# Performance work log

Hardware: AMD Instinct MI355X
Metric: run time of the kernel (lower is better)

The kernel has to match this reference:

```python
import jax, jax.numpy as jnp
import numpy as np
from jax import lax

N = 64          # n (even -> odd=0, add_odd=0)
B = 256         # batch
F = 256         # input_features
ITERS = 10      # sinkhorn iterations


def _conv1d(x, w, b, pad, dil):
    # x: (B, Cin, L), w: (Cout, Cin, K) torch layout
    y = lax.conv_general_dilated(
        x, w, window_strides=(1,), padding=[(pad, pad)],
        rhs_dilation=(dil,), dimension_numbers=("NCH", "OIH", "NCH"))
    return y + b[None, :, None]


def setup_inputs() -> dict:
    key = jax.random.key(0)
    ks = jax.random.split(key, 17)
    s = 0.02
    d = {
        "x": jax.random.normal(ks[0], (B, F), jnp.float32),
        # linear stack (torch Linear layout: (out, in))
        "w1": jax.random.normal(ks[1], (2 * N, F), jnp.float32) * s,
        "b1": jax.random.normal(ks[2], (2 * N,), jnp.float32) * s,
        "w2": jax.random.normal(ks[3], (N * N, 2 * N), jnp.float32) * s,
        "b2": jax.random.normal(ks[4], (N * N,), jnp.float32) * s,
        "w3": jax.random.normal(ks[5], (4 * N * N, N * N), jnp.float32) * s,
        "b3": jax.random.normal(ks[6], (4 * N * N,), jnp.float32) * s,
        # conv stack: 2n->3n->2n->n->n->n, all k=3
        "cw1": jax.random.normal(ks[7], (3 * N, 2 * N, 3), jnp.float32) * s,
        "cb1": jax.random.normal(ks[8], (3 * N,), jnp.float32) * s,
        "cw2": jax.random.normal(ks[9], (2 * N, 3 * N, 3), jnp.float32) * s,
        "cb2": jax.random.normal(ks[10], (2 * N,), jnp.float32) * s,
        "cw3": jax.random.normal(ks[11], (N, 2 * N, 3), jnp.float32) * s,
        "cb3": jax.random.normal(ks[12], (N,), jnp.float32) * s,
        "cw4": jax.random.normal(ks[13], (N, N, 3), jnp.float32) * s,
        "cb4": jax.random.normal(ks[14], (N,), jnp.float32) * s,
        "cw5": jax.random.normal(ks[15], (N, N, 3), jnp.float32) * s,
        "cb5": jax.random.normal(ks[16], (N,), jnp.float32) * s,
    }
    return d


def _sink(x, iters):
    # output = x + 0.001; repeat: row-normalize then col-normalize
    out = x + 0.001

    def body(o, _):
        o = o / jnp.sum(o, axis=2, keepdims=True)  # row_sink: divide each row by its sum
        o = o / jnp.sum(o, axis=1, keepdims=True)  # col_sink: divide each column by its sum
        return o, None

    out, _ = lax.scan(body, out, None, length=iters)
    return out


def reference(x, w1, b1, w2, b2, w3, b3,
              cw1, cb1, cw2, cb2, cw3, cb3, cw4, cb4, cw5, cb5):
    h = x @ w1.T + b1
    h = h @ w2.T + b2
    h = h @ w3.T + b3                      # (B, 4n^2)
    h = h.reshape(B, 2 * N, 2 * N)         # (B, 128, 128)
    # conv1: p=0, d=(n-8)//2=28 (since n>10); rest pad=0, dil=1
    h = _conv1d(h, cw1, cb1, 0, (N - 8) // 2)  # (B, 192, 72)
    h = _conv1d(h, cw2, cb2, 0, 1)             # (B, 128, 70)
    h = _conv1d(h, cw3, cb3, 0, 1)             # (B, 64, 68)
    h = _conv1d(h, cw4, cb4, 0, 1)             # (B, 64, 66)
    h = _conv1d(h, cw5, cb5, 0, 1)             # (B, 64, 64)
    h = h * h                                   # torch.pow(x, 2)
    return _sink(h, ITERS)
```

## Files before the change

kernel.cpp:

```cpp
#include <hip/hip_runtime.h>
#include <hip/hip_bf16.h>

typedef float f32x4 __attribute__((ext_vector_type(4)));
typedef __bf16 bf16x8 __attribute__((ext_vector_type(8)));

__global__ __launch_bounds__(128) void gemm1_k(const float* __restrict__ x,
                                               const float* __restrict__ w1,
                                               const float* __restrict__ b1,
                                               float* __restrict__ h1) {
    __shared__ float xs[256];
    const int m = blockIdx.x, t = threadIdx.x;
    xs[t] = x[m * 256 + t];
    xs[t + 128] = x[m * 256 + 128 + t];
    __syncthreads();
    float acc = b1[t];
    const float4* wr = (const float4*)(w1 + t * 256);
#pragma unroll 8
    for (int k4 = 0; k4 < 64; ++k4) {
        float4 w = wr[k4];
        acc += xs[k4 * 4 + 0] * w.x + xs[k4 * 4 + 1] * w.y +
               xs[k4 * 4 + 2] * w.z + xs[k4 * 4 + 3] * w.w;
    }
    h1[m * 128 + t] = acc;
}

__global__ __launch_bounds__(256) void gemm2_k(const float* __restrict__ h1,
                                               const float* __restrict__ w2,
                                               const float* __restrict__ b2,
                                               float* __restrict__ h2) {
    __shared__ float As[64][129];
    __shared__ float Bs[64][129];
    const int nb = blockIdx.x, mb = blockIdx.y, t = threadIdx.x;
#pragma unroll
    for (int i = 0; i < 8; ++i) {
        int idx = i * 256 + t;
        int row = idx >> 5, c4 = (idx & 31) * 4;
        float4 a = *(const float4*)(h1 + (mb * 64 + row) * 128 + c4);
        As[row][c4 + 0] = a.x; As[row][c4 + 1] = a.y;
        As[row][c4 + 2] = a.z; As[row][c4 + 3] = a.w;
        float4 bv = *(const float4*)(w2 + (nb * 64 + row) * 128 + c4);
        Bs[row][c4 + 0] = bv.x; Bs[row][c4 + 1] = bv.y;
        Bs[row][c4 + 2] = bv.z; Bs[row][c4 + 3] = bv.w;
    }
    __syncthreads();
    const int tx = t & 15, ty = t >> 4;
    float acc[4][4] = {};
#pragma unroll 4
    for (int k = 0; k < 128; ++k) {
        float a[4], b[4];
#pragma unroll
        for (int i = 0; i < 4; ++i) a[i] = As[ty * 4 + i][k];
#pragma unroll
        for (int j = 0; j < 4; ++j) b[j] = Bs[tx * 4 + j][k];
#pragma unroll
        for (int i = 0; i < 4; ++i)
#pragma unroll
            for (int j = 0; j < 4; ++j) acc[i][j] += a[i] * b[j];
    }
#pragma unroll
    for (int i = 0; i < 4; ++i)
#pragma unroll
        for (int j = 0; j < 4; ++j) {
            int n = nb * 64 + tx * 4 + j;
            h2[(mb * 64 + ty * 4 + i) * 4096 + n] = acc[i][j] + b2[n];
        }
}

__device__ __forceinline__ void g3_load(const float* __restrict__ A,
                                        const float* __restrict__ W,
                                        int n0, int k0, int tid,
                                        float4 (&ar)[4][2], float4 (&wr)[2]) {
    const int kb = tid & 7, mrow = tid >> 3;
#pragma unroll
    for (int i = 0; i < 4; ++i) {
        const float* p = A + (i * 64 + mrow) * 4096 + k0 + kb * 8;
        ar[i][0] = *(const float4*)p;
        ar[i][1] = *(const float4*)(p + 4);
    }
    const float* q = W + (n0 + mrow) * 4096 + k0 + kb * 8;
    wr[0] = *(const float4*)q;
    wr[1] = *(const float4*)(q + 4);
}

__device__ __forceinline__ bf16x8 pack8(const float4& lo, const float4& hi) {
    bf16x8 p;
    p[0] = (__bf16)lo.x; p[1] = (__bf16)lo.y; p[2] = (__bf16)lo.z; p[3] = (__bf16)lo.w;
    p[4] = (__bf16)hi.x; p[5] = (__bf16)hi.y; p[6] = (__bf16)hi.z; p[7] = (__bf16)hi.w;
    return p;
}

__device__ __forceinline__ void g3_store(char* Ab, char* Wb, int tid,
                                         const float4 (&ar)[4][2],
                                         const float4 (&wr)[2]) {
    const int kb = tid & 7, mrow = tid >> 3;
#pragma unroll
    for (int i = 0; i < 4; ++i) {
        int m = i * 64 + mrow;
        *(bf16x8*)(Ab + ((m * 128 + kb * 16) ^ ((m & 7) << 4))) = pack8(ar[i][0], ar[i][1]);
    }
    *(bf16x8*)(Wb + ((mrow * 128 + kb * 16) ^ ((mrow & 7) << 4))) = pack8(wr[0], wr[1]);
}

__global__ __launch_bounds__(512, 1) void gemm3_k(const float* __restrict__ A,
                                                  const float* __restrict__ W,
                                                  const float* __restrict__ bias,
                                                  float* __restrict__ C) {
    __shared__ __align__(16) char lds[81920];
    const int tid = threadIdx.x;
    const int n0 = blockIdx.x * 64;

    float4 ar[4][2];
    float4 wr[2];
    g3_load(A, W, n0, 0, tid, ar, wr);
    g3_store(lds, lds + 65536, tid, ar, wr);
    __syncthreads();

    const int lane = tid & 63, wid = tid >> 6;
    const int lr = lane & 15, lq = lane >> 4;
    const int wm = wid >> 1, wn = wid & 1;

    f32x4 acc[4][2];
    const f32x4 zero = {0.f, 0.f, 0.f, 0.f};
#pragma unroll
    for (int mi = 0; mi < 4; ++mi)
#pragma unroll
        for (int ni = 0; ni < 2; ++ni) acc[mi][ni] = zero;

    for (int t = 0; t < 64; ++t) {
        const int cur = t & 1;
        if (t < 63) g3_load(A, W, n0, (t + 1) * 64, tid, ar, wr);
        const char* Ac = lds + cur * 32768;
        const char* Wc = lds + 65536 + cur * 8192;
#pragma unroll
        for (int kk = 0; kk < 2; ++kk) {
            const int kb = kk * 4 + lq;
            bf16x8 af[4], bfv[2];
#pragma unroll
            for (int mi = 0; mi < 4; ++mi) {
                int m = wm * 64 + mi * 16 + lr;
                af[mi] = *(const bf16x8*)(Ac + ((m * 128 + kb * 16) ^ ((m & 7) << 4)));
            }
#pragma unroll
            for (int ni = 0; ni < 2; ++ni) {
                int n = wn * 32 + ni * 16 + lr;
                bfv[ni] = *(const bf16x8*)(Wc + ((n * 128 + kb * 16) ^ ((n & 7) << 4)));
            }
#pragma unroll
            for (int mi = 0; mi < 4; ++mi)
#pragma unroll
                for (int ni = 0; ni < 2; ++ni)
                    acc[mi][ni] = __builtin_amdgcn_mfma_f32_16x16x32_bf16(
                        af[mi], bfv[ni], acc[mi][ni], 0, 0, 0);
        }
        __syncthreads();
        if (t < 63)
            g3_store(lds + (cur ^ 1) * 32768, lds + 65536 + (cur ^ 1) * 8192,
                     tid, ar, wr);
        __syncthreads();
    }

    float bv[2];
#pragma unroll
    for (int ni = 0; ni < 2; ++ni) bv[ni] = bias[n0 + wn * 32 + ni * 16 + lr];
#pragma unroll
    for (int mi = 0; mi < 4; ++mi)
#pragma unroll
        for (int ni = 0; ni < 2; ++ni) {
            const int n = n0 + wn * 32 + ni * 16 + lr;
#pragma unroll
            for (int r = 0; r < 4; ++r) {
                int m = wm * 64 + mi * 16 + lq * 4 + r;
                C[m * 16384 + n] = acc[mi][ni][r] + bv[ni];
            }
        }
}

template <int CIN, int COUT, int DIL, int MT, int NT>
__device__ __forceinline__ void conv_core(const char* xt, char* wl,
                                          const float* __restrict__ w,
                                          f32x4 (&acc)[MT][NT], int tid) {
    constexpr int RB = CIN * 2;
    const int lane = tid & 63, wid = tid >> 6;
    const int lr = lane & 15, lq = lane >> 4;
    const int cobase = wid * (COUT / 4);
    const f32x4 zero = {0.f, 0.f, 0.f, 0.f};
#pragma unroll
    for (int mi = 0; mi < MT; ++mi)
#pragma unroll
        for (int ni = 0; ni < NT; ++ni) acc[mi][ni] = zero;

    for (int cic = 0; cic < CIN / 32; ++cic) {
        for (int idx = tid; idx < COUT * 4; idx += 256) {
            int co = idx >> 2, cib = idx & 3, ci0 = cic * 32 + cib * 8;
            const float* src = w + co * (CIN * 3) + ci0 * 3;
            float v[24];
#pragma unroll
            for (int u = 0; u < 6; ++u) {
                float4 f = *(const float4*)(src + u * 4);
                v[u * 4 + 0] = f.x; v[u * 4 + 1] = f.y;
                v[u * 4 + 2] = f.z; v[u * 4 + 3] = f.w;
            }
#pragma unroll
            for (int tp = 0; tp < 3; ++tp) {
                bf16x8 pk;
#pragma unroll
                for (int j = 0; j < 8; ++j) pk[j] = (__bf16)v[j * 3 + tp];
                *(bf16x8*)(wl + ((tp * 4 + cib) * COUT + co) * 16) = pk;
            }
        }
        __syncthreads();
#pragma unroll
        for (int tp = 0; tp < 3; ++tp) {
            bf16x8 af[MT];
#pragma unroll
            for (int mi = 0; mi < MT; ++mi)
                af[mi] = *(const bf16x8*)(wl + ((tp * 4 + lq) * COUT + cobase + mi * 16 + lr) * 16);
            bf16x8 bfr[NT];
#pragma unroll
            for (int ni = 0; ni < NT; ++ni) {
                int colX = ni * 16 + lr + tp * DIL;
                bfr[ni] = *(const bf16x8*)(xt + ((colX * RB + (cic * 4 + lq) * 16) ^ ((colX & 7) << 4)));
            }
#pragma unroll
            for (int mi = 0; mi < MT; ++mi)
#pragma unroll
                for (int ni = 0; ni < NT; ++ni)
                    acc[mi][ni] = __builtin_amdgcn_mfma_f32_16x16x32_bf16(
                        af[mi], bfr[ni], acc[mi][ni], 0, 0, 0);
        }
        __syncthreads();
    }
}

template <int COUT, int LOUT, int MT, int NT>
__device__ __forceinline__ void write_xt(char* xt_out, const f32x4 (&acc)[MT][NT],
                                         const float* __restrict__ bias, int tid) {
    constexpr int RBO = COUT * 2;
    const int lane = tid & 63, wid = tid >> 6;
    const int lr = lane & 15, lq = lane >> 4;
    const int cobase = wid * (COUT / 4);
#pragma unroll
    for (int mi = 0; mi < MT; ++mi)
#pragma unroll
        for (int ni = 0; ni < NT; ++ni) {
            int l = ni * 16 + lr;
            if (l < LOUT) {
#pragma unroll
                for (int r = 0; r < 4; ++r) {
                    int co = cobase + mi * 16 + lq * 4 + r;
                    float y = acc[mi][ni][r] + bias[co];
                    int byte = (l * RBO + ((co >> 3) << 4) + (co & 7) * 2) ^ ((l & 7) << 4);
                    *(__bf16*)(xt_out + byte) = (__bf16)y;
                }
            }
        }
}

__global__ __launch_bounds__(256, 1) void convsink_k(
    const float* __restrict__ h3,
    const float* __restrict__ cw1, const float* __restrict__ cb1,
    const float* __restrict__ cw2, const float* __restrict__ cb2,
    const float* __restrict__ cw3, const float* __restrict__ cb3,
    const float* __restrict__ cw4, const float* __restrict__ cb4,
    const float* __restrict__ cw5, const float* __restrict__ cb5,
    float* __restrict__ out) {
    __shared__ __align__(16) char lds[34816 + 31488 + 36864 + 16640];
    char* xtA = lds;
    char* xtB = lds + 34816;
    char* wl = lds + 34816 + 31488;
    float* S = (float*)(lds + 34816 + 31488 + 36864);

    const int b = blockIdx.x, tid = threadIdx.x;
    const float* src = h3 + b * 16384;

#pragma unroll
    for (int i = 0; i < 8; ++i) {
        int idx = i * 256 + tid;
        int l = idx & 127, cib = idx >> 7;
        bf16x8 p;
#pragma unroll
        for (int j = 0; j < 8; ++j) p[j] = (__bf16)src[(cib * 8 + j) * 128 + l];
        *(bf16x8*)(xtA + ((l * 256 + cib * 16) ^ ((l & 7) << 4))) = p;
    }
    __syncthreads();

    {
        f32x4 acc[3][5];
        conv_core<128, 192, 28, 3, 5>(xtA, wl, cw1, acc, tid);
        write_xt<192, 72, 3, 5>(xtB, acc, cb1, tid);
    }
    __syncthreads();
    {
        f32x4 acc[2][5];
        conv_core<192, 128, 1, 2, 5>(xtB, wl, cw2, acc, tid);
        write_xt<128, 70, 2, 5>(xtA, acc, cb2, tid);
    }
    __syncthreads();
    {
        f32x4 acc[1][5];
        conv_core<128, 64, 1, 1, 5>(xtA, wl, cw3, acc, tid);
        write_xt<64, 68, 1, 5>(xtB, acc, cb3, tid);
    }
    __syncthreads();
    {
        f32x4 acc[1][5];
        conv_core<64, 64, 1, 1, 5>(xtB, wl, cw4, acc, tid);
        write_xt<64, 66, 1, 5>(xtA, acc, cb4, tid);
    }
    __syncthreads();
    {
        f32x4 acc[1][4];
        conv_core<64, 64, 1, 1, 4>(xtA, wl, cw5, acc, tid);
        const int lane = tid & 63, wid = tid >> 6;
        const int lr = lane & 15, lq = lane >> 4;
        const int cobase = wid * 16;
#pragma unroll
        for (int ni = 0; ni < 4; ++ni) {
            int l = ni * 16 + lr;
#pragma unroll
            for (int r = 0; r < 4; ++r) {
                int co = cobase + lq * 4 + r;
                float y = acc[0][ni][r] + cb5[co];
                S[co * 65 + l] = y * y + 0.001f;
            }
        }
    }
    __syncthreads();

    const int q = tid & 3, rid = tid >> 2;
    for (int it = 0; it < 10; ++it) {
        float p = 0.f;
#pragma unroll
        for (int j = 0; j < 16; ++j) p += S[rid * 65 + q * 16 + j];
        p += __shfl_xor(p, 1);
        p += __shfl_xor(p, 2);
        float inv = 1.0f / p;
#pragma unroll
        for (int j = 0; j < 16; ++j) S[rid * 65 + q * 16 + j] *= inv;
        __syncthreads();
        float c = 0.f;
#pragma unroll
        for (int i = 0; i < 16; ++i) c += S[(q * 16 + i) * 65 + rid];
        c += __shfl_xor(c, 1);
        c += __shfl_xor(c, 2);
        float invc = 1.0f / c;
#pragma unroll
        for (int i = 0; i < 16; ++i) S[(q * 16 + i) * 65 + rid] *= invc;
        __syncthreads();
    }

#pragma unroll
    for (int i = 0; i < 16; ++i) {
        int idx = i * 256 + tid;
        out[b * 4096 + idx] = S[(idx >> 6) * 65 + (idx & 63)];
    }
}

extern "C" void kernel_launch(void* const* d_in, const int* in_sizes, int n_in,
                              void* d_out, int out_size, void* d_ws, size_t ws_size,
                              hipStream_t stream) {
    const float* x = (const float*)d_in[0];
    const float* w1 = (const float*)d_in[1];
    const float* b1 = (const float*)d_in[2];
    const float* w2 = (const float*)d_in[3];
    const float* b2 = (const float*)d_in[4];
    const float* w3 = (const float*)d_in[5];
    const float* b3 = (const float*)d_in[6];
    const float* cw1 = (const float*)d_in[7];
    const float* cb1 = (const float*)d_in[8];
    const float* cw2 = (const float*)d_in[9];
    const float* cb2 = (const float*)d_in[10];
    const float* cw3 = (const float*)d_in[11];
    const float* cb3 = (const float*)d_in[12];
    const float* cw4 = (const float*)d_in[13];
    const float* cb4 = (const float*)d_in[14];
    const float* cw5 = (const float*)d_in[15];
    const float* cb5 = (const float*)d_in[16];
    float* out = (float*)d_out;

    char* ws = (char*)d_ws;
    float* h1 = (float*)(ws);
    float* h2 = (float*)(ws + 131072);
    float* h3 = (float*)(ws + 131072 + 4194304);

    gemm1_k<<<256, 128, 0, stream>>>(x, w1, b1, h1);
    gemm2_k<<<dim3(64, 4), 256, 0, stream>>>(h1, w2, b2, h2);
    gemm3_k<<<256, 512, 0, stream>>>(h2, w3, b3, h3);
    convsink_k<<<256, 256, 0, stream>>>(h3, cw1, cb1, cw2, cb2, cw3, cb3,
                                        cw4, cb4, cw5, cb5, out);
}
```

Baseline: 160.8 us.

## Store gemm2 output as pre-swizzled bf16 and stream it into LDS directly

```diff
diff --git a/kernel.cpp b/kernel.cpp
--- a/kernel.cpp
+++ b/kernel.cpp
@@ -3,6 +3,9 @@
 
 typedef float f32x4 __attribute__((ext_vector_type(4)));
 typedef __bf16 bf16x8 __attribute__((ext_vector_type(8)));
+
+typedef __attribute__((address_space(1))) const unsigned int as1_uint;
+typedef __attribute__((address_space(3))) unsigned int as3_uint;
 
 __global__ __launch_bounds__(128) void gemm1_k(const float* __restrict__ x,
                                                const float* __restrict__ w1,
@@ -27,7 +30,7 @@
 __global__ __launch_bounds__(256) void gemm2_k(const float* __restrict__ h1,
                                                const float* __restrict__ w2,
                                                const float* __restrict__ b2,
-                                               float* __restrict__ h2) {
+                                               char* __restrict__ h2b) {
     __shared__ float As[64][129];
     __shared__ float Bs[64][129];
     const int nb = blockIdx.x, mb = blockIdx.y, t = threadIdx.x;
@@ -61,61 +64,55 @@
     for (int i = 0; i < 4; ++i)
 #pragma unroll
         for (int j = 0; j < 4; ++j) {
+            int m = mb * 64 + ty * 4 + i;
             int n = nb * 64 + tx * 4 + j;
-            h2[(mb * 64 + ty * 4 + i) * 4096 + n] = acc[i][j] + b2[n];
-        }
-}
-
-__device__ __forceinline__ void g3_load(const float* __restrict__ A,
-                                        const float* __restrict__ W,
-                                        int n0, int k0, int tid,
-                                        float4 (&ar)[4][2], float4 (&wr)[2]) {
-    const int kb = tid & 7, mrow = tid >> 3;
-#pragma unroll
-    for (int i = 0; i < 4; ++i) {
-        const float* p = A + (i * 64 + mrow) * 4096 + k0 + kb * 8;
-        ar[i][0] = *(const float4*)p;
-        ar[i][1] = *(const float4*)(p + 4);
-    }
-    const float* q = W + (n0 + mrow) * 4096 + k0 + kb * 8;
-    wr[0] = *(const float4*)q;
-    wr[1] = *(const float4*)(q + 4);
-}
-
-__device__ __forceinline__ bf16x8 pack8(const float4& lo, const float4& hi) {
-    bf16x8 p;
-    p[0] = (__bf16)lo.x; p[1] = (__bf16)lo.y; p[2] = (__bf16)lo.z; p[3] = (__bf16)lo.w;
-    p[4] = (__bf16)hi.x; p[5] = (__bf16)hi.y; p[6] = (__bf16)hi.z; p[7] = (__bf16)hi.w;
-    return p;
-}
-
-__device__ __forceinline__ void g3_store(char* Ab, char* Wb, int tid,
-                                         const float4 (&ar)[4][2],
-                                         const float4 (&wr)[2]) {
-    const int kb = tid & 7, mrow = tid >> 3;
-#pragma unroll
-    for (int i = 0; i < 4; ++i) {
-        int m = i * 64 + mrow;
-        *(bf16x8*)(Ab + ((m * 128 + kb * 16) ^ ((m & 7) << 4))) = pack8(ar[i][0], ar[i][1]);
-    }
-    *(bf16x8*)(Wb + ((mrow * 128 + kb * 16) ^ ((mrow & 7) << 4))) = pack8(wr[0], wr[1]);
-}
-
-__global__ __launch_bounds__(512, 1) void gemm3_k(const float* __restrict__ A,
+            float v = acc[i][j] + b2[n];
+            int kb = n >> 6, r = n & 63;
+            int byte = kb * 32768 + ((m * 128 + (r >> 3) * 16) ^ ((m & 7) << 4)) + (r & 7) * 2;
+            *(__bf16*)(h2b + byte) = (__bf16)v;
+        }
+}
+
+__global__ __launch_bounds__(512, 1) void gemm3_k(const char* __restrict__ Ab,
                                                   const float* __restrict__ W,
                                                   const float* __restrict__ bias,
                                                   float* __restrict__ C) {
     __shared__ __align__(16) char lds[81920];
     const int tid = threadIdx.x;
     const int n0 = blockIdx.x * 64;
-
-    float4 ar[4][2];
-    float4 wr[2];
-    g3_load(A, W, n0, 0, tid, ar, wr);
-    g3_store(lds, lds + 65536, tid, ar, wr);
-    __syncthreads();
-
     const int lane = tid & 63, wid = tid >> 6;
+    const int mrow = tid >> 3, kb8 = tid & 7;
+
+#define ISSUE_A(t, buf)                                                          \
+    {                                                                            \
+        const char* _s = Ab + (t) * 32768 + wid * 4096 + lane * 16;              \
+        char* _d = lds + (buf) * 32768 + wid * 4096;                             \
+        __builtin_amdgcn_global_load_lds((as1_uint*)(_s), (as3_uint*)(_d), 16, 0, 0);          \
+        __builtin_amdgcn_global_load_lds((as1_uint*)(_s + 1024), (as3_uint*)(_d + 1024), 16, 0, 0); \
+        __builtin_amdgcn_global_load_lds((as1_uint*)(_s + 2048), (as3_uint*)(_d + 2048), 16, 0, 0); \
+        __builtin_amdgcn_global_load_lds((as1_uint*)(_s + 3072), (as3_uint*)(_d + 3072), 16, 0, 0); \
+    }
+
+    float4 w0, w1;
+    auto loadW = [&](int t) {
+        const float* q = W + (n0 + mrow) * 4096 + t * 64 + kb8 * 8;
+        w0 = *(const float4*)q;
+        w1 = *(const float4*)(q + 4);
+    };
+    auto storeW = [&](int buf) {
+        bf16x8 p;
+        p[0] = (__bf16)w0.x; p[1] = (__bf16)w0.y; p[2] = (__bf16)w0.z; p[3] = (__bf16)w0.w;
+        p[4] = (__bf16)w1.x; p[5] = (__bf16)w1.y; p[6] = (__bf16)w1.z; p[7] = (__bf16)w1.w;
+        *(bf16x8*)(lds + 65536 + buf * 8192 +
+                   ((mrow * 128 + kb8 * 16) ^ ((mrow & 7) << 4))) = p;
+    };
+
+    ISSUE_A(0, 0);
+    loadW(0);
+    __syncthreads();
+    storeW(0);
+    __syncthreads();
+
     const int lr = lane & 15, lq = lane >> 4;
     const int wm = wid >> 1, wn = wid & 1;
 
@@ -128,7 +125,10 @@
 
     for (int t = 0; t < 64; ++t) {
         const int cur = t & 1;
-        if (t < 63) g3_load(A, W, n0, (t + 1) * 64, tid, ar, wr);
+        if (t < 63) {
+            ISSUE_A(t + 1, cur ^ 1);
+            loadW(t + 1);
+        }
         const char* Ac = lds + cur * 32768;
         const char* Wc = lds + 65536 + cur * 8192;
 #pragma unroll
@@ -153,11 +153,10 @@
                         af[mi], bfv[ni], acc[mi][ni], 0, 0, 0);
         }
         __syncthreads();
-        if (t < 63)
-            g3_store(lds + (cur ^ 1) * 32768, lds + 65536 + (cur ^ 1) * 8192,
-                     tid, ar, wr);
-        __syncthreads();
-    }
+        if (t < 63) storeW(cur ^ 1);
+        __syncthreads();
+    }
+#undef ISSUE_A
 
     float bv[2];
 #pragma unroll
@@ -380,12 +379,12 @@
 
     char* ws = (char*)d_ws;
     float* h1 = (float*)(ws);
-    float* h2 = (float*)(ws + 131072);
-    float* h3 = (float*)(ws + 131072 + 4194304);
+    char* h2b = ws + 131072;
+    float* h3 = (float*)(ws + 131072 + 2097152);
 
     gemm1_k<<<256, 128, 0, stream>>>(x, w1, b1, h1);
-    gemm2_k<<<dim3(64, 4), 256, 0, stream>>>(h1, w2, b2, h2);
-    gemm3_k<<<256, 512, 0, stream>>>(h2, w3, b3, h3);
+    gemm2_k<<<dim3(64, 4), 256, 0, stream>>>(h1, w2, b2, h2b);
+    gemm3_k<<<256, 512, 0, stream>>>(h2b, w3, b3, h3);
     convsink_k<<<256, 256, 0, stream>>>(h3, cw1, cb1, cw2, cb2, cw3, cb3,
                                         cw4, cb4, cw5, cb5, out);
 }
```

After: 150.1 us. 6.6% less time.
